# Kernel optimization log

Hardware: AMD Instinct MI355X
Metric: run time of the kernel (lower is better)

The kernel has to match this reference:

```python
import jax, jax.numpy as jnp
import numpy as np

N, E, HEADS = 50000, 800000, 4
IN_C, HID_C, OUT_C = 128, 64, 40
WIDTH = HEADS * HID_C  # 256
NEG_SLOPE = 0.2
BN_EPS = 1e-5


def setup_inputs() -> dict:
    key = jax.random.key(0)
    ks = jax.random.split(key, 16)
    s = 0.05
    inp = {
        "x": jax.random.normal(ks[0], (N, IN_C), jnp.float32),
        "edge_index": jax.random.randint(ks[1], (2, E), 0, N, jnp.int32),
        # layer 0: in -> (heads, hid), concat
        "W0": jax.random.normal(ks[2], (IN_C, WIDTH), jnp.float32) * s,
        "a_src0": jax.random.normal(ks[3], (HEADS, HID_C), jnp.float32) * s,
        "a_dst0": jax.random.normal(ks[4], (HEADS, HID_C), jnp.float32) * s,
        "b0": jnp.zeros((WIDTH,), jnp.float32),
        "g0": jnp.ones((WIDTH,), jnp.float32),
        "beta0": jnp.zeros((WIDTH,), jnp.float32),
        # layer 1: width -> (heads, hid), concat
        "W1": jax.random.normal(ks[5], (WIDTH, WIDTH), jnp.float32) * s,
        "a_src1": jax.random.normal(ks[6], (HEADS, HID_C), jnp.float32) * s,
        "a_dst1": jax.random.normal(ks[7], (HEADS, HID_C), jnp.float32) * s,
        "b1": jnp.zeros((WIDTH,), jnp.float32),
        "g1": jnp.ones((WIDTH,), jnp.float32),
        "beta1": jnp.zeros((WIDTH,), jnp.float32),
        # layer 2: width -> (heads, out), mean over heads (concat=False)
        "W2": jax.random.normal(ks[8], (WIDTH, HEADS * OUT_C), jnp.float32) * s,
        "a_src2": jax.random.normal(ks[9], (HEADS, OUT_C), jnp.float32) * s,
        "a_dst2": jax.random.normal(ks[10], (HEADS, OUT_C), jnp.float32) * s,
        "b2": jnp.zeros((OUT_C,), jnp.float32),
    }
    return inp


def _gat_layer(x, W, a_src, a_dst, b, src, dst, out_c, concat):
    # x: [N, F_in]; W: [F_in, HEADS*out_c]
    h = (x @ W).reshape(N, HEADS, out_c)              # [N, H, C]
    e_src = jnp.sum(h * a_src, axis=-1)               # [N, H]
    e_dst = jnp.sum(h * a_dst, axis=-1)               # [N, H]
    e = jax.nn.leaky_relu(e_src[src] + e_dst[dst], NEG_SLOPE)  # [E', H]
    # segment softmax over incoming edges of each destination node
    m = jax.ops.segment_max(e, dst, num_segments=N)
    e = jnp.exp(e - m[dst])
    z = jax.ops.segment_sum(e, dst, num_segments=N)
    alpha = e / (z[dst] + 1e-16)                      # [E', H]
    msg = h[src] * alpha[:, :, None]                  # [E', H, C]
    out = jax.ops.segment_sum(msg, dst, num_segments=N)  # [N, H, C]
    if concat:
        return out.reshape(N, HEADS * out_c) + b
    return out.mean(axis=1) + b


def _batchnorm(x, g, beta):
    mu = x.mean(axis=0)
    var = x.var(axis=0)
    return (x - mu) * jax.lax.rsqrt(var + BN_EPS) * g + beta


def reference(x, edge_index, W0, a_src0, a_dst0, b0, g0, beta0,
              W1, a_src1, a_dst1, b1, g1, beta1,
              W2, a_src2, a_dst2, b2):
    # add self-loops (PyG GATConv default)
    loops = jnp.arange(N, dtype=edge_index.dtype)
    src = jnp.concatenate([edge_index[0], loops])
    dst = jnp.concatenate([edge_index[1], loops])

    h = _gat_layer(x, W0, a_src0, a_dst0, b0, src, dst, HID_C, True)
    h = jax.nn.elu(_batchnorm(h, g0, beta0))
    h = _gat_layer(h, W1, a_src1, a_dst1, b1, src, dst, HID_C, True)
    h = jax.nn.elu(_batchnorm(h, g1, beta1))
    h = _gat_layer(h, W2, a_src2, a_dst2, b2, src, dst, OUT_C, False)
    return jax.nn.log_softmax(h, axis=-1)
```

## Files before the change

### kernel.cpp

```cpp
#include <hip/hip_runtime.h>

#define NN 50000
#define EE 800000
#define NEP (EE + NN)
#define NBS 512
#define SCB 49

typedef float f32x4 __attribute__((ext_vector_type(4)));
typedef float f32x2 __attribute__((ext_vector_type(2)));
typedef short bf16x8 __attribute__((ext_vector_type(8)));

__device__ inline float bf2f(unsigned short u) {
    union { unsigned int i; float f; } v; v.i = ((unsigned int)u) << 16; return v.f;
}
__device__ inline float lo2f(unsigned int u) {
    return __builtin_bit_cast(float, u << 16);
}
__device__ inline float hi2f(unsigned int u) {
    return __builtin_bit_cast(float, u & 0xFFFF0000u);
}
__device__ inline unsigned short f2bf(float f) {
    unsigned int x = __builtin_bit_cast(unsigned int, f);
    unsigned int r = x + 0x7FFFu + ((x >> 16) & 1u);
    return (unsigned short)(r >> 16);
}

__global__ __launch_bounds__(256) void k_cs(const int* __restrict__ ei,
                                            int* __restrict__ counts, int* __restrict__ lps) {
    int e = blockIdx.x * 256 + threadIdx.x;
    if (e >= NEP) return;
    int dst = (e < EE) ? ei[EE + e] : (e - EE);
    lps[e] = atomicAdd(&counts[dst], 1);
}

__global__ __launch_bounds__(256) void k_scan1(const int* __restrict__ counts,
                                               int* __restrict__ indptr, int* __restrict__ bsum) {
    const int tid = threadIdx.x, lane = tid & 63, wid = tid >> 6;
    const int base = blockIdx.x * 1024 + tid * 4;
    int4 v = make_int4(0, 0, 0, 0);
    if (base + 3 < NN) v = *(const int4*)&counts[base];
    else {
        if (base + 0 < NN) v.x = counts[base + 0];
        if (base + 1 < NN) v.y = counts[base + 1];
        if (base + 2 < NN) v.z = counts[base + 2];
        if (base + 3 < NN) v.w = counts[base + 3];
    }
    int t = v.x + v.y + v.z + v.w;
    int s = t;
    #pragma unroll
    for (int d = 1; d < 64; d <<= 1) { int u = __shfl_up(s, d); if (lane >= d) s += u; }
    __shared__ int ws[4], wo[4];
    if (lane == 63) ws[wid] = s;
    __syncthreads();
    if (tid == 0) {
        int a = 0;
        #pragma unroll
        for (int j = 0; j < 4; j++) { wo[j] = a; a += ws[j]; }
        bsum[blockIdx.x] = a;
    }
    __syncthreads();
    int excl = wo[wid] + s - t;
    int p0 = excl, p1 = p0 + v.x, p2 = p1 + v.y, p3 = p2 + v.z;
    if (base + 3 < NN) *(int4*)&indptr[base] = make_int4(p0, p1, p2, p3);
    else {
        if (base + 0 < NN) indptr[base + 0] = p0;
        if (base + 1 < NN) indptr[base + 1] = p1;
        if (base + 2 < NN) indptr[base + 2] = p2;
        if (base + 3 < NN) indptr[base + 3] = p3;
    }
}

__global__ __launch_bounds__(64) void k_scan2(int* __restrict__ bsum, int* __restrict__ indptr) {
    const int lane = threadIdx.x;
    int v = (lane < SCB) ? bsum[lane] : 0;
    int s = v;
    #pragma unroll
    for (int d = 1; d < 64; d <<= 1) { int u = __shfl_up(s, d); if (lane >= d) s += u; }
    if (lane < SCB) bsum[lane] = s - v;
    if (lane == SCB - 1) indptr[NN] = s;
}

__global__ __launch_bounds__(256) void k_scan3(int* __restrict__ indptr, const int* __restrict__ bsum) {
    const int base = blockIdx.x * 1024 + threadIdx.x * 4;
    const int off = bsum[blockIdx.x];
    if (off == 0) return;
    if (base + 3 < NN) {
        int4 v = *(const int4*)&indptr[base];
        v.x += off; v.y += off; v.z += off; v.w += off;
        *(int4*)&indptr[base] = v;
    } else {
        #pragma unroll
        for (int j = 0; j < 4; j++)
            if (base + j < NN) indptr[base + j] += off;
    }
}

__global__ __launch_bounds__(256) void k_place(const int* __restrict__ ei,
                                               const int* __restrict__ indptr,
                                               const int* __restrict__ lps,
                                               int* __restrict__ srcs) {
    int e = blockIdx.x * 256 + threadIdx.x;
    if (e >= NEP) return;
    int src, dst;
    if (e < EE) { src = ei[e]; dst = ei[EE + e]; }
    else        { src = e - EE; dst = src; }
    srcs[indptr[dst] + lps[e]] = src;
}

__global__ __launch_bounds__(256) void k_expand(const int* __restrict__ indptr,
                                                int* __restrict__ dstc) {
    const int wid = threadIdx.x >> 6, lane = threadIdx.x & 63;
    const int n = blockIdx.x * 4 + wid;
    if (n >= NN) return;
    const int e0 = __builtin_amdgcn_readfirstlane(indptr[n]);
    const int e1 = __builtin_amdgcn_readfirstlane(indptr[n + 1]);
    for (int e = e0 + lane; e < e1; e += 64) dstc[e] = n;
}

#define XN4 1600000
__global__ __launch_bounds__(256) void k_prep(const float* __restrict__ x, unsigned short* __restrict__ xb,
        const float* __restrict__ W0, unsigned short* __restrict__ Wt0,
        const float* __restrict__ W1, unsigned short* __restrict__ Wt1,
        const float* __restrict__ W2, unsigned short* __restrict__ Wt2,
        const float* __restrict__ vs0, const float* __restrict__ vd0,
        float4* __restrict__ es4, float4* __restrict__ ed4) {
    int i = blockIdx.x * 256 + threadIdx.x;
    if (i < XN4) {
        float4 v = ((const float4*)x)[i];
        ushort4 o;
        o.x = f2bf(v.x); o.y = f2bf(v.y); o.z = f2bf(v.z); o.w = f2bf(v.w);
        ((ushort4*)xb)[i] = o;
        const int k0 = (i & 31) * 4;
        const float vv[4] = {v.x, v.y, v.z, v.w};
        float s[4] = {0.f, 0.f, 0.f, 0.f}, dd[4] = {0.f, 0.f, 0.f, 0.f};
        #pragma unroll
        for (int j = 0; j < 4; j++) {
            float f = vv[j];
            float4 a = *(const float4*)&vs0[(k0 + j) * 4];
            float4 b = *(const float4*)&vd0[(k0 + j) * 4];
            s[0] += f * a.x; s[1] += f * a.y; s[2] += f * a.z; s[3] += f * a.w;
            dd[0] += f * b.x; dd[1] += f * b.y; dd[2] += f * b.z; dd[3] += f * b.w;
        }
        #pragma unroll
        for (int d = 1; d < 32; d <<= 1) {
            #pragma unroll
            for (int j = 0; j < 4; j++) { s[j] += __shfl_xor(s[j], d); dd[j] += __shfl_xor(dd[j], d); }
        }
        if ((threadIdx.x & 31) == 0) {
            int row = i >> 5;
            es4[row] = make_float4(s[0], s[1], s[2], s[3]);
            ed4[row] = make_float4(dd[0], dd[1], dd[2], dd[3]);
        }
        return;
    }
    i -= XN4;
    if (i < 256 * 128) {
        int c = i >> 7, k = i & 127;
        Wt0[i] = f2bf(W0[(size_t)k * 256 + c]);
        return;
    }
    i -= 256 * 128;
    if (i < 256 * 256) {
        int c = i >> 8, k = i & 255;
        Wt1[i] = f2bf(W1[(size_t)k * 256 + c]);
        return;
    }
    i -= 256 * 256;
    if (i < 192 * 256) {
        int c = i >> 8, k = i & 255;
        Wt2[i] = f2bf((c < 160) ? W2[(size_t)k * 160 + c] : 0.f);
    }
}

__global__ __launch_bounds__(256) void k_wv(
        const float* __restrict__ W0, const float* __restrict__ as0, const float* __restrict__ ad0,
        const float* __restrict__ W1, const float* __restrict__ as1, const float* __restrict__ ad1,
        const float* __restrict__ W2, const float* __restrict__ as2, const float* __restrict__ ad2,
        float* __restrict__ vs0, float* __restrict__ vd0,
        float* __restrict__ vs1, float* __restrict__ vd1,
        float* __restrict__ vs2, float* __restrict__ vd2) {
    int b = blockIdx.x;
    const float *W, *as_, *ad_; float *vs, *vd; int k, C, NO;
    if (b < 128)      { W = W0; as_ = as0; ad_ = ad0; vs = vs0; vd = vd0; k = b;       C = 64; NO = 256; }
    else if (b < 384) { W = W1; as_ = as1; ad_ = ad1; vs = vs1; vd = vd1; k = b - 128; C = 64; NO = 256; }
    else              { W = W2; as_ = as2; ad_ = ad2; vs = vs2; vd = vd2; k = b - 384; C = 40; NO = 160; }
    int h = threadIdx.x >> 6, c = threadIdx.x & 63;
    float s1 = 0.f, s2 = 0.f;
    if (c < C) {
        float wv = W[(size_t)k * NO + h * C + c];
        s1 = wv * as_[h * C + c];
        s2 = wv * ad_[h * C + c];
    }
    #pragma unroll
    for (int d = 1; d < 64; d <<= 1) { s1 += __shfl_xor(s1, d); s2 += __shfl_xor(s2, d); }
    if (c == 0) { vs[k * 4 + h] = s1; vd[k * 4 + h] = s2; }
}

__global__ __launch_bounds__(256) void k_wgt(const float4* __restrict__ es4,
        const float4* __restrict__ ed4, const int* __restrict__ srcs,
        const int* __restrict__ dstc, float* __restrict__ wqf) {
    int p = blockIdx.x * 256 + threadIdx.x;
    if (p >= NEP) return;
    float4 s = es4[srcs[p]];
    float4 d = ed4[dstc[p]];
    float e0 = s.x + d.x, e1 = s.y + d.y, e2 = s.z + d.z, e3 = s.w + d.w;
    e0 = (e0 > 0.f) ? e0 : 0.2f * e0;
    e1 = (e1 > 0.f) ? e1 : 0.2f * e1;
    e2 = (e2 > 0.f) ? e2 : 0.2f * e2;
    e3 = (e3 > 0.f) ? e3 : 0.2f * e3;
    wqf[p]            = __expf(e0);
    wqf[NEP + p]      = __expf(e1);
    wqf[2 * NEP + p]  = __expf(e2);
    wqf[3 * NEP + p]  = __expf(e3);
}

template<int K, int NOUTP, int NO>
__global__ __launch_bounds__(256) void k_gemm(const unsigned short* __restrict__ Xb,
                                              const unsigned short* __restrict__ Wt,
                                              unsigned char* __restrict__ Y) {
    constexpr int G = K / 8;
    __shared__ __attribute__((aligned(16))) unsigned short As[64 * K];
    const int bm = blockIdx.x * 64;
    const int tid = threadIdx.x, lane = tid & 63, wid = tid >> 6;
    const int wm = wid >> 1, wn = wid & 1;
    const int l15 = lane & 15, l4 = lane >> 4;

    #pragma unroll
    for (int i = 0; i < (64 * G) / 256; i++) {
        int p = tid + 256 * i;
        int row = p / G, g = p % G;
        int grow = bm + row; if (grow >= NN) grow = 0;
        int gsrc = g ^ (row & 7);
        const unsigned short* gp = &Xb[(size_t)grow * K + gsrc * 8];
        __builtin_amdgcn_global_load_lds(
            (const __attribute__((address_space(1))) void*)gp,
            (__attribute__((address_space(3))) void*)&As[p * 8],
            16, 0, 0);
    }
    __syncthreads();

    #pragma unroll
    for (int bg = 0; bg < NOUTP / 64; bg++) {
        const int bn = bg * 64;
        bf16x8 bfr[2][K / 32];
        #pragma unroll
        for (int n = 0; n < 2; n++) {
            const int col = bn + wn * 32 + n * 16 + l15;
            #pragma unroll
            for (int ks = 0; ks < K / 32; ks++)
                bfr[n][ks] = *(const bf16x8*)&Wt[(size_t)col * K + ks * 32 + l4 * 8];
        }
        f32x4 acc[2][2];
        #pragma unroll
        for (int m = 0; m < 2; m++)
            #pragma unroll
            for (int n = 0; n < 2; n++) acc[m][n] = (f32x4)0.f;
        #pragma unroll
        for (int ks = 0; ks < K / 32; ks++) {
            #pragma unroll
            for (int m = 0; m < 2; m++) {
                const int r = wm * 32 + m * 16 + l15;
                const int pg = ((ks << 2) + l4) ^ (r & 7);
                bf16x8 af = *(const bf16x8*)&As[r * K + pg * 8];
                #pragma unroll
                for (int n = 0; n < 2; n++)
                    acc[m][n] = __builtin_amdgcn_mfma_f32_16x16x32_bf16(af, bfr[n][ks], acc[m][n], 0, 0, 0);
            }
        }
        #pragma unroll
        for (int m = 0; m < 2; m++) {
            const int row0 = bm + wm * 32 + m * 16 + l4 * 4;
            #pragma unroll
            for (int n = 0; n < 2; n++) {
                const int col = bn + wn * 32 + n * 16 + l15;
                if (col >= NO) continue;
                #pragma unroll
                for (int j = 0; j < 4; j++) {
                    int gr = row0 + j;
                    if (gr >= NN) continue;
                    int pk = __builtin_amdgcn_cvt_pk_fp8_f32(acc[m][n][j], acc[m][n][j], 0, false);
                    Y[(size_t)gr * NOUTP + col] = (unsigned char)pk;
                }
            }
        }
    }
}

__global__ __launch_bounds__(256) void k_agg(const unsigned char* __restrict__ H,
        const float* __restrict__ wqf,
        const int* __restrict__ indptr, const int* __restrict__ srcs,
        unsigned short* __restrict__ outp) {
    const int wid = threadIdx.x >> 6, lane = threadIdx.x & 63;
    const int n = blockIdx.x * 4 + wid;
    if (n >= NN) return;
    const int head = lane >> 4;
    const float* __restrict__ wh = wqf + (size_t)head * NEP;
    const int e0 = __builtin_amdgcn_readfirstlane(indptr[n]);
    const int e1 = __builtin_amdgcn_readfirstlane(indptr[n + 1]);
    float z = 0.f, a0 = 0.f, a1 = 0.f, a2 = 0.f, a3 = 0.f;
    const unsigned char* Hp = H + lane * 4;
    int e = e0;
    for (; e + 8 <= e1; e += 8) {
        int s[8]; float ww[8];
        #pragma unroll
        for (int q = 0; q < 8; q++) { s[q] = srcs[e + q]; ww[q] = wh[e + q]; }
        #pragma unroll
        for (int q = 0; q < 8; q++) {
            unsigned int hv = *(const unsigned int*)(Hp + (size_t)s[q] * 256);
            z += ww[q];
            f32x2 lo = __builtin_amdgcn_cvt_pk_f32_fp8(hv, false);
            f32x2 hi = __builtin_amdgcn_cvt_pk_f32_fp8(hv, true);
            a0 += ww[q] * lo[0]; a1 += ww[q] * lo[1];
            a2 += ww[q] * hi[0]; a3 += ww[q] * hi[1];
        }
    }
    for (; e < e1; ++e) {
        int s0 = srcs[e];
        float w0 = wh[e];
        unsigned int hv = *(const unsigned int*)(Hp + (size_t)s0 * 256);
        z += w0;
        f32x2 lo = __builtin_amdgcn_cvt_pk_f32_fp8(hv, false);
        f32x2 hi = __builtin_amdgcn_cvt_pk_f32_fp8(hv, true);
        a0 += w0 * lo[0]; a1 += w0 * lo[1];
        a2 += w0 * hi[0]; a3 += w0 * hi[1];
    }
    float inv = 1.f / (z + 1e-16f);
    ushort4 o;
    o.x = f2bf(a0 * inv); o.y = f2bf(a1 * inv); o.z = f2bf(a2 * inv); o.w = f2bf(a3 * inv);
    *(ushort4*)&outp[(size_t)n * 256 + lane * 4] = o;
}

__global__ __launch_bounds__(256) void k_agg2(const unsigned char* __restrict__ H2,
        const float* __restrict__ wqf,
        const int* __restrict__ indptr, const int* __restrict__ srcs,
        const float* __restrict__ b2, float* __restrict__ outp) {
    const int wid = threadIdx.x >> 6, lane = threadIdx.x & 63;
    const int n = blockIdx.x * 4 + wid;
    if (n >= NN) return;
    const bool act = lane < 40;
    const int head = lane / 10;
    const float* __restrict__ wh = wqf + (size_t)(act ? head : 0) * NEP;
    const int e0 = __builtin_amdgcn_readfirstlane(indptr[n]);
    const int e1 = __builtin_amdgcn_readfirstlane(indptr[n + 1]);
    float z = 0.f, acc[4] = {0.f, 0.f, 0.f, 0.f};
    const unsigned char* Hp = H2 + lane * 4;
    if (act) {
        int e = e0;
        for (; e + 8 <= e1; e += 8) {
            int s[8]; float ww[8];
            #pragma unroll
            for (int q = 0; q < 8; q++) { s[q] = srcs[e + q]; ww[q] = wh[e + q]; }
            #pragma unroll
            for (int q = 0; q < 8; q++) {
                unsigned int hv = *(const unsigned int*)(Hp + (size_t)s[q] * 192);
                z += ww[q];
                f32x2 lo = __builtin_amdgcn_cvt_pk_f32_fp8(hv, false);
                f32x2 hi = __builtin_amdgcn_cvt_pk_f32_fp8(hv, true);
                acc[0] += ww[q] * lo[0]; acc[1] += ww[q] * lo[1];
                acc[2] += ww[q] * hi[0]; acc[3] += ww[q] * hi[1];
            }
        }
        for (; e < e1; ++e) {
            int s0 = srcs[e];
            float w0 = wh[e];
            unsigned int hv = *(const unsigned int*)(Hp + (size_t)s0 * 192);
            z += w0;
            f32x2 lo = __builtin_amdgcn_cvt_pk_f32_fp8(hv, false);
            f32x2 hi = __builtin_amdgcn_cvt_pk_f32_fp8(hv, true);
            acc[0] += w0 * lo[0]; acc[1] += w0 * lo[1];
            acc[2] += w0 * hi[0]; acc[3] += w0 * hi[1];
        }
    }
    float inv = 1.f / (z + 1e-16f);
    float sv[4];
    #pragma unroll
    for (int j = 0; j < 4; j++) sv[j] = acc[j] * inv;
    #pragma unroll
    for (int j = 0; j < 4; j++) {
        float v = sv[j];
        v += __shfl(sv[j], lane + 10);
        v += __shfl(sv[j], lane + 20);
        v += __shfl(sv[j], lane + 30);
        sv[j] = v;
    }
    const bool ol = lane < 10;
    float m4 = -1e30f;
    #pragma unroll
    for (int j = 0; j < 4; j++) {
        sv[j] = ol ? (0.25f * sv[j] + b2[lane * 4 + j]) : -1e30f;
        m4 = fmaxf(m4, sv[j]);
    }
    #pragma unroll
    for (int d = 1; d < 16; d <<= 1) m4 = fmaxf(m4, __shfl_xor(m4, d));
    float s = 0.f;
    #pragma unroll
    for (int j = 0; j < 4; j++) s += ol ? __expf(sv[j] - m4) : 0.f;
    #pragma unroll
    for (int d = 1; d < 16; d <<= 1) s += __shfl_xor(s, d);
    float ls = logf(s);
    if (ol) {
        float4 o = make_float4(sv[0] - m4 - ls, sv[1] - m4 - ls, sv[2] - m4 - ls, sv[3] - m4 - ls);
        *(float4*)&outp[(size_t)n * 40 + lane * 4] = o;
    }
}

__global__ __launch_bounds__(256) void k_bnstats1(const unsigned short* __restrict__ X,
        float* __restrict__ ps, float* __restrict__ pq) {
    __shared__ float lds[4 * 256];
    const int tid = threadIdx.x;
    const int colg = (tid & 63) * 4;
    const int w = tid >> 6;
    float s[4] = {0.f, 0.f, 0.f, 0.f}, q[4] = {0.f, 0.f, 0.f, 0.f};
    for (int r = blockIdx.x * 4 + w; r < NN; r += NBS * 4) {
        ushort4 hv = *(const ushort4*)&X[(size_t)r * 256 + colg];
        const unsigned short hh[4] = {hv.x, hv.y, hv.z, hv.w};
        #pragma unroll
        for (int j = 0; j < 4; j++) { float v = bf2f(hh[j]); s[j] += v; q[j] += v * v; }
    }
    #pragma unroll
    for (int j = 0; j < 4; j++) lds[w * 256 + colg + j] = s[j];
    __syncthreads();
    float ts = lds[tid] + lds[256 + tid] + lds[512 + tid] + lds[768 + tid];
    __syncthreads();
    #pragma unroll
    for (int j = 0; j < 4; j++) lds[w * 256 + colg + j] = q[j];
    __syncthreads();
    float tq = lds[tid] + lds[256 + tid] + lds[512 + tid] + lds[768 + tid];
    ps[(size_t)blockIdx.x * 256 + tid] = ts;
    pq[(size_t)blockIdx.x * 256 + tid] = tq;
}

__global__ __launch_bounds__(256) void k_bnred(const float* __restrict__ ps,
        const float* __restrict__ pq, const float* __restrict__ g,
        const float* __restrict__ beta, float* __restrict__ sc_o, float* __restrict__ sh_o) {
    const int col = blockIdx.x, tid = threadIdx.x;
    float s = ps[(size_t)tid * 256 + col] + ps[(size_t)(tid + 256) * 256 + col];
    float q = pq[(size_t)tid * 256 + col] + pq[(size_t)(tid + 256) * 256 + col];
    #pragma unroll
    for (int d = 1; d < 64; d <<= 1) { s += __shfl_xor(s, d); q += __shfl_xor(q, d); }
    __shared__ float ls[4], lq[4];
    if ((tid & 63) == 0) { ls[tid >> 6] = s; lq[tid >> 6] = q; }
    __syncthreads();
    if (tid == 0) {
        float S = ls[0] + ls[1] + ls[2] + ls[3];
        float Q = lq[0] + lq[1] + lq[2] + lq[3];
        const float inv = 1.f / (float)NN;
        float mu = S * inv;
        float var = Q * inv - mu * mu;
        float sc = rsqrtf(var + 1e-5f) * g[col];
        sc_o[col] = sc;
        sh_o[col] = beta[col] - mu * sc;
    }
}

__global__ __launch_bounds__(256) void k_bnapply(unsigned short* __restrict__ X,
        const float* __restrict__ sc_i, const float* __restrict__ sh_i,
        const float* __restrict__ vs, const float* __restrict__ vd,
        float4* __restrict__ es4, float4* __restrict__ ed4) {
    const int hl = threadIdx.x & 31;
    const int colg = hl * 8;
    const int rowo = threadIdx.x >> 5;
    float sc[8], sh[8];
    #pragma unroll
    for (int j = 0; j < 8; j++) { sc[j] = sc_i[colg + j]; sh[j] = sh_i[colg + j]; }
    for (int r = blockIdx.x * 8 + rowo; r < NN; r += gridDim.x * 8) {
        uint4 u = *(uint4*)&X[(size_t)r * 256 + colg];
        unsigned int uu[4] = {u.x, u.y, u.z, u.w};
        unsigned int oo[4];
        float s[4] = {0.f, 0.f, 0.f, 0.f}, dd[4] = {0.f, 0.f, 0.f, 0.f};
        #pragma unroll
        for (int p = 0; p < 4; p++) {
            float lo = lo2f(uu[p]);
            float hi = hi2f(uu[p]);
            float vlo = lo * sc[p * 2] + sh[p * 2];
            float vhi = hi * sc[p * 2 + 1] + sh[p * 2 + 1];
            vlo = (vlo > 0.f) ? vlo : expm1f(vlo);
            vhi = (vhi > 0.f) ? vhi : expm1f(vhi);
            oo[p] = (unsigned int)f2bf(vlo) | ((unsigned int)f2bf(vhi) << 16);
            float4 a0 = *(const float4*)&vs[(colg + 2 * p) * 4];
            float4 b0 = *(const float4*)&vd[(colg + 2 * p) * 4];
            float4 a1 = *(const float4*)&vs[(colg + 2 * p + 1) * 4];
            float4 b1 = *(const float4*)&vd[(colg + 2 * p + 1) * 4];
            s[0] += vlo * a0.x + vhi * a1.x; s[1] += vlo * a0.y + vhi * a1.y;
            s[2] += vlo * a0.z + vhi * a1.z; s[3] += vlo * a0.w + vhi * a1.w;
            dd[0] += vlo * b0.x + vhi * b1.x; dd[1] += vlo * b0.y + vhi * b1.y;
            dd[2] += vlo * b0.z + vhi * b1.z; dd[3] += vlo * b0.w + vhi * b1.w;
        }
        *(uint4*)&X[(size_t)r * 256 + colg] = make_uint4(oo[0], oo[1], oo[2], oo[3]);
        #pragma unroll
        for (int d = 1; d < 32; d <<= 1) {
            #pragma unroll
            for (int j = 0; j < 4; j++) { s[j] += __shfl_xor(s[j], d); dd[j] += __shfl_xor(dd[j], d); }
        }
        if (hl == 0) {
            es4[r] = make_float4(s[0], s[1], s[2], s[3]);
            ed4[r] = make_float4(dd[0], dd[1], dd[2], dd[3]);
        }
    }
}

extern "C" void kernel_launch(void* const* d_in, const int* in_sizes, int n_in,
                              void* d_out, int out_size, void* d_ws, size_t ws_size,
                              hipStream_t stream) {
    const float* x   = (const float*)d_in[0];
    const int*   ei  = (const int*)d_in[1];
    const float* W0  = (const float*)d_in[2];
    const float* as0 = (const float*)d_in[3];
    const float* ad0 = (const float*)d_in[4];
    const float* g0  = (const float*)d_in[6];
    const float* be0 = (const float*)d_in[7];
    const float* W1  = (const float*)d_in[8];
    const float* as1 = (const float*)d_in[9];
    const float* ad1 = (const float*)d_in[10];
    const float* g1  = (const float*)d_in[12];
    const float* be1 = (const float*)d_in[13];
    const float* W2  = (const float*)d_in[14];
    const float* as2 = (const float*)d_in[15];
    const float* ad2 = (const float*)d_in[16];
    const float* b2  = (const float*)d_in[17];
    float* out = (float*)d_out;

    char* w = (char*)d_ws;
    size_t off = 0;
    auto take = [&](size_t bytes) -> void* {
        off = (off + 255) & ~(size_t)255;
        void* p = w + off; off += bytes; return p;
    };
    unsigned short* Agg16 = (unsigned short*)take((size_t)NN * 256 * 2);
    unsigned short* xb    = (unsigned short*)take((size_t)NN * 128 * 2);
    unsigned char*  H8    = (unsigned char*)take((size_t)NN * 256);
    float* es     = (float*)take((size_t)NN * 4 * 4);
    float* ed     = (float*)take((size_t)NN * 4 * 4);
    int*   counts = (int*)take((size_t)NN * 4);
    int*   indptr = (int*)take((size_t)(NN + 1) * 4);
    int*   lps    = (int*)take((size_t)NEP * 4);
    int*   srcs   = (int*)take((size_t)NEP * 4);
    int*   dstc   = (int*)take((size_t)NEP * 4);
    float* wqf    = (float*)take((size_t)NEP * 4 * 4);
    int*   bsum   = (int*)take(64 * 4);
    unsigned short* Wt0 = (unsigned short*)take((size_t)256 * 128 * 2);
    unsigned short* Wt1 = (unsigned short*)take((size_t)256 * 256 * 2);
    unsigned short* Wt2 = (unsigned short*)take((size_t)192 * 256 * 2);
    float* vs0 = (float*)take(128 * 4 * 4);
    float* vd0 = (float*)take(128 * 4 * 4);
    float* vs1 = (float*)take(256 * 4 * 4);
    float* vd1 = (float*)take(256 * 4 * 4);
    float* vs2 = (float*)take(256 * 4 * 4);
    float* vd2 = (float*)take(256 * 4 * 4);
    float* ps  = (float*)take((size_t)NBS * 256 * 4);
    float* pq  = (float*)take((size_t)NBS * 256 * 4);
    float* bns = (float*)take(512 * 4);

    const int gE = (NEP + 255) / 256;
    const int gPrep = (XN4 + 256 * 128 + 256 * 256 + 192 * 256 + 255) / 256;

    k_wv<<<640, 256, 0, stream>>>(W0, as0, ad0, W1, as1, ad1, W2, as2, ad2,
                                  vs0, vd0, vs1, vd1, vs2, vd2);
    k_prep<<<gPrep, 256, 0, stream>>>(x, xb, W0, Wt0, W1, Wt1, W2, Wt2,
                                      vs0, vd0, (float4*)es, (float4*)ed);

    hipMemsetAsync(counts, 0, (size_t)NN * 4, stream);
    k_cs   <<<gE, 256, 0, stream>>>(ei, counts, lps);
    k_scan1<<<SCB, 256, 0, stream>>>(counts, indptr, bsum);
    k_scan2<<<1, 64, 0, stream>>>(bsum, indptr);
    k_scan3<<<SCB, 256, 0, stream>>>(indptr, bsum);
    k_place<<<gE, 256, 0, stream>>>(ei, indptr, lps, srcs);

    const int gM = (NN + 63) / 64;
    const int gW = (NN + 3) / 4;

    k_expand<<<gW, 256, 0, stream>>>(indptr, dstc);

    k_wgt<<<gE, 256, 0, stream>>>((const float4*)es, (const float4*)ed, srcs, dstc, wqf);
    k_gemm<128, 256, 256><<<gM, 256, 0, stream>>>(xb, Wt0, H8);
    k_agg<<<gW, 256, 0, stream>>>(H8, wqf, indptr, srcs, Agg16);
    k_bnstats1<<<NBS, 256, 0, stream>>>(Agg16, ps, pq);
    k_bnred<<<256, 256, 0, stream>>>(ps, pq, g0, be0, bns, bns + 256);
    k_bnapply<<<1024, 256, 0, stream>>>(Agg16, bns, bns + 256, vs1, vd1,
                                        (float4*)es, (float4*)ed);

    k_wgt<<<gE, 256, 0, stream>>>((const float4*)es, (const float4*)ed, srcs, dstc, wqf);
    k_gemm<256, 256, 256><<<gM, 256, 0, stream>>>(Agg16, Wt1, H8);
    k_agg<<<gW, 256, 0, stream>>>(H8, wqf, indptr, srcs, Agg16);
    k_bnstats1<<<NBS, 256, 0, stream>>>(Agg16, ps, pq);
    k_bnred<<<256, 256, 0, stream>>>(ps, pq, g1, be1, bns, bns + 256);
    k_bnapply<<<1024, 256, 0, stream>>>(Agg16, bns, bns + 256, vs2, vd2,
                                        (float4*)es, (float4*)ed);

    k_wgt<<<gE, 256, 0, stream>>>((const float4*)es, (const float4*)ed, srcs, dstc, wqf);
    k_gemm<256, 192, 160><<<gM, 256, 0, stream>>>(Agg16, Wt2, H8);
    k_agg2<<<gW, 256, 0, stream>>>(H8, wqf, indptr, srcs, b2, out);
}
```

Measured before the change: 381.5 us.

## Merge independent kernels via block-range dispatch and pack edge weights as bf16

```diff
diff --git a/kernel.cpp b/kernel.cpp
--- a/kernel.cpp
+++ b/kernel.cpp
@@ -25,12 +25,72 @@
     return (unsigned short)(r >> 16);
 }
 
-__global__ __launch_bounds__(256) void k_cs(const int* __restrict__ ei,
-                                            int* __restrict__ counts, int* __restrict__ lps) {
-    int e = blockIdx.x * 256 + threadIdx.x;
-    if (e >= NEP) return;
-    int dst = (e < EE) ? ei[EE + e] : (e - EE);
-    lps[e] = atomicAdd(&counts[dst], 1);
+#define XN4 1600000
+#define GPREP 6826
+#define GEDGE 3321
+#define GWAVE 12500
+#define GMAT  782
+
+__global__ __launch_bounds__(256) void k_prep(const float* __restrict__ x, unsigned short* __restrict__ xb,
+        const float* __restrict__ W0, unsigned short* __restrict__ Wt0,
+        const float* __restrict__ W1, unsigned short* __restrict__ Wt1,
+        const float* __restrict__ W2, unsigned short* __restrict__ Wt2,
+        const float* __restrict__ vs0, const float* __restrict__ vd0,
+        float4* __restrict__ es4, float4* __restrict__ ed4,
+        const int* __restrict__ ei, int* __restrict__ counts, int* __restrict__ lps) {
+    if (blockIdx.x >= GPREP) {
+        int e = (blockIdx.x - GPREP) * 256 + threadIdx.x;
+        if (e >= NEP) return;
+        int dst = (e < EE) ? ei[EE + e] : (e - EE);
+        lps[e] = atomicAdd(&counts[dst], 1);
+        return;
+    }
+    int i = blockIdx.x * 256 + threadIdx.x;
+    if (i < XN4) {
+        float4 v = ((const float4*)x)[i];
+        ushort4 o;
+        o.x = f2bf(v.x); o.y = f2bf(v.y); o.z = f2bf(v.z); o.w = f2bf(v.w);
+        ((ushort4*)xb)[i] = o;
+        const int k0 = (i & 31) * 4;
+        const float vv[4] = {v.x, v.y, v.z, v.w};
+        float s[4] = {0.f, 0.f, 0.f, 0.f}, dd[4] = {0.f, 0.f, 0.f, 0.f};
+        #pragma unroll
+        for (int j = 0; j < 4; j++) {
+            float f = vv[j];
+            float4 a = *(const float4*)&vs0[(k0 + j) * 4];
+            float4 b = *(const float4*)&vd0[(k0 + j) * 4];
+            s[0] += f * a.x; s[1] += f * a.y; s[2] += f * a.z; s[3] += f * a.w;
+            dd[0] += f * b.x; dd[1] += f * b.y; dd[2] += f * b.z; dd[3] += f * b.w;
+        }
+        #pragma unroll
+        for (int d = 1; d < 32; d <<= 1) {
+            #pragma unroll
+            for (int j = 0; j < 4; j++) { s[j] += __shfl_xor(s[j], d); dd[j] += __shfl_xor(dd[j], d); }
+        }
+        if ((threadIdx.x & 31) == 0) {
+            int row = i >> 5;
+            es4[row] = make_float4(s[0], s[1], s[2], s[3]);
+            ed4[row] = make_float4(dd[0], dd[1], dd[2], dd[3]);
+        }
+        return;
+    }
+    i -= XN4;
+    if (i < 256 * 128) {
+        int c = i >> 7, k = i & 127;
+        Wt0[i] = f2bf(W0[(size_t)k * 256 + c]);
+        return;
+    }
+    i -= 256 * 128;
+    if (i < 256 * 256) {
+        int c = i >> 8, k = i & 255;
+        Wt1[i] = f2bf(W1[(size_t)k * 256 + c]);
+        return;
+    }
+    i -= 256 * 256;
+    if (i < 192 * 256) {
+        int c = i >> 8, k = i & 255;
+        Wt2[i] = f2bf((c < 160) ? W2[(size_t)k * 160 + c] : 0.f);
+    }
 }
 
 __global__ __launch_bounds__(256) void k_scan1(const int* __restrict__ counts,
@@ -98,78 +158,23 @@
 __global__ __launch_bounds__(256) void k_place(const int* __restrict__ ei,
                                                const int* __restrict__ indptr,
                                                const int* __restrict__ lps,
-                                               int* __restrict__ srcs) {
-    int e = blockIdx.x * 256 + threadIdx.x;
-    if (e >= NEP) return;
-    int src, dst;
-    if (e < EE) { src = ei[e]; dst = ei[EE + e]; }
-    else        { src = e - EE; dst = src; }
-    srcs[indptr[dst] + lps[e]] = src;
-}
-
-__global__ __launch_bounds__(256) void k_expand(const int* __restrict__ indptr,
-                                                int* __restrict__ dstc) {
+                                               int* __restrict__ srcs,
+                                               int* __restrict__ dstc) {
+    if (blockIdx.x < GEDGE) {
+        int e = blockIdx.x * 256 + threadIdx.x;
+        if (e >= NEP) return;
+        int src, dst;
+        if (e < EE) { src = ei[e]; dst = ei[EE + e]; }
+        else        { src = e - EE; dst = src; }
+        srcs[indptr[dst] + lps[e]] = src;
+        return;
+    }
     const int wid = threadIdx.x >> 6, lane = threadIdx.x & 63;
-    const int n = blockIdx.x * 4 + wid;
+    const int n = (blockIdx.x - GEDGE) * 4 + wid;
     if (n >= NN) return;
     const int e0 = __builtin_amdgcn_readfirstlane(indptr[n]);
     const int e1 = __builtin_amdgcn_readfirstlane(indptr[n + 1]);
     for (int e = e0 + lane; e < e1; e += 64) dstc[e] = n;
-}
-
-#define XN4 1600000
-__global__ __launch_bounds__(256) void k_prep(const float* __restrict__ x, unsigned short* __restrict__ xb,
-        const float* __restrict__ W0, unsigned short* __restrict__ Wt0,
-        const float* __restrict__ W1, unsigned short* __restrict__ Wt1,
-        const float* __restrict__ W2, unsigned short* __restrict__ Wt2,
-        const float* __restrict__ vs0, const float* __restrict__ vd0,
-        float4* __restrict__ es4, float4* __restrict__ ed4) {
-    int i = blockIdx.x * 256 + threadIdx.x;
-    if (i < XN4) {
-        float4 v = ((const float4*)x)[i];
-        ushort4 o;
-        o.x = f2bf(v.x); o.y = f2bf(v.y); o.z = f2bf(v.z); o.w = f2bf(v.w);
-        ((ushort4*)xb)[i] = o;
-        const int k0 = (i & 31) * 4;
-        const float vv[4] = {v.x, v.y, v.z, v.w};
-        float s[4] = {0.f, 0.f, 0.f, 0.f}, dd[4] = {0.f, 0.f, 0.f, 0.f};
-        #pragma unroll
-        for (int j = 0; j < 4; j++) {
-            float f = vv[j];
-            float4 a = *(const float4*)&vs0[(k0 + j) * 4];
-            float4 b = *(const float4*)&vd0[(k0 + j) * 4];
-            s[0] += f * a.x; s[1] += f * a.y; s[2] += f * a.z; s[3] += f * a.w;
-            dd[0] += f * b.x; dd[1] += f * b.y; dd[2] += f * b.z; dd[3] += f * b.w;
-        }
-        #pragma unroll
-        for (int d = 1; d < 32; d <<= 1) {
-            #pragma unroll
-            for (int j = 0; j < 4; j++) { s[j] += __shfl_xor(s[j], d); dd[j] += __shfl_xor(dd[j], d); }
-        }
-        if ((threadIdx.x & 31) == 0) {
-            int row = i >> 5;
-            es4[row] = make_float4(s[0], s[1], s[2], s[3]);
-            ed4[row] = make_float4(dd[0], dd[1], dd[2], dd[3]);
-        }
-        return;
-    }
-    i -= XN4;
-    if (i < 256 * 128) {
-        int c = i >> 7, k = i & 127;
-        Wt0[i] = f2bf(W0[(size_t)k * 256 + c]);
-        return;
-    }
-    i -= 256 * 128;
-    if (i < 256 * 256) {
-        int c = i >> 8, k = i & 255;
-        Wt1[i] = f2bf(W1[(size_t)k * 256 + c]);
-        return;
-    }
-    i -= 256 * 256;
-    if (i < 192 * 256) {
-        int c = i >> 8, k = i & 255;
-        Wt2[i] = f2bf((c < 160) ? W2[(size_t)k * 160 + c] : 0.f);
-    }
 }
 
 __global__ __launch_bounds__(256) void k_wv(
@@ -196,28 +201,31 @@
     if (c == 0) { vs[k * 4 + h] = s1; vd[k * 4 + h] = s2; }
 }
 
-__global__ __launch_bounds__(256) void k_wgt(const float4* __restrict__ es4,
-        const float4* __restrict__ ed4, const int* __restrict__ srcs,
-        const int* __restrict__ dstc, float* __restrict__ wqf) {
-    int p = blockIdx.x * 256 + threadIdx.x;
-    if (p >= NEP) return;
-    float4 s = es4[srcs[p]];
-    float4 d = ed4[dstc[p]];
-    float e0 = s.x + d.x, e1 = s.y + d.y, e2 = s.z + d.z, e3 = s.w + d.w;
-    e0 = (e0 > 0.f) ? e0 : 0.2f * e0;
-    e1 = (e1 > 0.f) ? e1 : 0.2f * e1;
-    e2 = (e2 > 0.f) ? e2 : 0.2f * e2;
-    e3 = (e3 > 0.f) ? e3 : 0.2f * e3;
-    wqf[p]            = __expf(e0);
-    wqf[NEP + p]      = __expf(e1);
-    wqf[2 * NEP + p]  = __expf(e2);
-    wqf[3 * NEP + p]  = __expf(e3);
-}
-
 template<int K, int NOUTP, int NO>
 __global__ __launch_bounds__(256) void k_gemm(const unsigned short* __restrict__ Xb,
                                               const unsigned short* __restrict__ Wt,
-                                              unsigned char* __restrict__ Y) {
+                                              unsigned char* __restrict__ Y,
+                                              const float4* __restrict__ es4,
+                                              const float4* __restrict__ ed4,
+                                              const int* __restrict__ srcs,
+                                              const int* __restrict__ dstc,
+                                              uint2* __restrict__ wq) {
+    if (blockIdx.x >= GMAT) {
+        int p = (blockIdx.x - GMAT) * 256 + threadIdx.x;
+        if (p >= NEP) return;
+        float4 s = es4[srcs[p]];
+        float4 d = ed4[dstc[p]];
+        float e0 = s.x + d.x, e1 = s.y + d.y, e2 = s.z + d.z, e3 = s.w + d.w;
+        e0 = (e0 > 0.f) ? e0 : 0.2f * e0;
+        e1 = (e1 > 0.f) ? e1 : 0.2f * e1;
+        e2 = (e2 > 0.f) ? e2 : 0.2f * e2;
+        e3 = (e3 > 0.f) ? e3 : 0.2f * e3;
+        uint2 o;
+        o.x = (unsigned int)f2bf(__expf(e0)) | ((unsigned int)f2bf(__expf(e1)) << 16);
+        o.y = (unsigned int)f2bf(__expf(e2)) | ((unsigned int)f2bf(__expf(e3)) << 16);
+        wq[p] = o;
+        return;
+    }
     constexpr int G = K / 8;
     __shared__ __attribute__((aligned(16))) unsigned short As[64 * K];
     const int bm = blockIdx.x * 64;
@@ -287,14 +295,14 @@
 }
 
 __global__ __launch_bounds__(256) void k_agg(const unsigned char* __restrict__ H,
-        const float* __restrict__ wqf,
+        const uint2* __restrict__ wq,
         const int* __restrict__ indptr, const int* __restrict__ srcs,
         unsigned short* __restrict__ outp) {
     const int wid = threadIdx.x >> 6, lane = threadIdx.x & 63;
     const int n = blockIdx.x * 4 + wid;
     if (n >= NN) return;
     const int head = lane >> 4;
-    const float* __restrict__ wh = wqf + (size_t)head * NEP;
+    const int hw = head >> 1, hs = (head & 1) * 16;
     const int e0 = __builtin_amdgcn_readfirstlane(indptr[n]);
     const int e1 = __builtin_amdgcn_readfirstlane(indptr[n + 1]);
     float z = 0.f, a0 = 0.f, a1 = 0.f, a2 = 0.f, a3 = 0.f;
@@ -303,7 +311,12 @@
     for (; e + 8 <= e1; e += 8) {
         int s[8]; float ww[8];
         #pragma unroll
-        for (int q = 0; q < 8; q++) { s[q] = srcs[e + q]; ww[q] = wh[e + q]; }
+        for (int q = 0; q < 8; q++) {
+            s[q] = srcs[e + q];
+            uint2 w2 = wq[e + q];
+            unsigned int wsv = hw ? w2.y : w2.x;
+            ww[q] = bf2f((unsigned short)(wsv >> hs));
+        }
         #pragma unroll
         for (int q = 0; q < 8; q++) {
             unsigned int hv = *(const unsigned int*)(Hp + (size_t)s[q] * 256);
@@ -316,7 +329,9 @@
     }
     for (; e < e1; ++e) {
         int s0 = srcs[e];
-        float w0 = wh[e];
+        uint2 w2 = wq[e];
+        unsigned int wsv = hw ? w2.y : w2.x;
+        float w0 = bf2f((unsigned short)(wsv >> hs));
         unsigned int hv = *(const unsigned int*)(Hp + (size_t)s0 * 256);
         z += w0;
         f32x2 lo = __builtin_amdgcn_cvt_pk_f32_fp8(hv, false);
@@ -331,7 +346,7 @@
 }
 
 __global__ __launch_bounds__(256) void k_agg2(const unsigned char* __restrict__ H2,
-        const float* __restrict__ wqf,
+        const uint2* __restrict__ wq,
         const int* __restrict__ indptr, const int* __restrict__ srcs,
         const float* __restrict__ b2, float* __restrict__ outp) {
     const int wid = threadIdx.x >> 6, lane = threadIdx.x & 63;
@@ -339,7 +354,7 @@
     if (n >= NN) return;
     const bool act = lane < 40;
     const int head = lane / 10;
-    const float* __restrict__ wh = wqf + (size_t)(act ? head : 0) * NEP;
+    const int hw = head >> 1, hs = (head & 1) * 16;
     const int e0 = __builtin_amdgcn_readfirstlane(indptr[n]);
     const int e1 = __builtin_amdgcn_readfirstlane(indptr[n + 1]);
     float z = 0.f, acc[4] = {0.f, 0.f, 0.f, 0.f};
@@ -349,7 +364,12 @@
         for (; e + 8 <= e1; e += 8) {
             int s[8]; float ww[8];
             #pragma unroll
-            for (int q = 0; q < 8; q++) { s[q] = srcs[e + q]; ww[q] = wh[e + q]; }
+            for (int q = 0; q < 8; q++) {
+                s[q] = srcs[e + q];
+                uint2 w2 = wq[e + q];
+                unsigned int wsv = hw ? w2.y : w2.x;
+                ww[q] = bf2f((unsigned short)(wsv >> hs));
+            }
             #pragma unroll
             for (int q = 0; q < 8; q++) {
                 unsigned int hv = *(const unsigned int*)(Hp + (size_t)s[q] * 192);
@@ -362,7 +382,9 @@
         }
         for (; e < e1; ++e) {
             int s0 = srcs[e];
-            float w0 = wh[e];
+            uint2 w2 = wq[e];
+            unsigned int wsv = hw ? w2.y : w2.x;
+            float w0 = bf2f((unsigned short)(wsv >> hs));
             unsigned int hv = *(const unsigned int*)(Hp + (size_t)s0 * 192);
             z += w0;
             f32x2 lo = __builtin_amdgcn_cvt_pk_f32_fp8(hv, false);
@@ -536,7 +558,7 @@
     int*   lps    = (int*)take((size_t)NEP * 4);
     int*   srcs   = (int*)take((size_t)NEP * 4);
     int*   dstc   = (int*)take((size_t)NEP * 4);
-    float* wqf    = (float*)take((size_t)NEP * 4 * 4);
+    uint2* wq     = (uint2*)take((size_t)NEP * 8);
     int*   bsum   = (int*)take(64 * 4);
     unsigned short* Wt0 = (unsigned short*)take((size_t)256 * 128 * 2);
     unsigned short* Wt1 = (unsigned short*)take((size_t)256 * 256 * 2);
@@ -551,43 +573,34 @@
     float* pq  = (float*)take((size_t)NBS * 256 * 4);
     float* bns = (float*)take(512 * 4);
 
-    const int gE = (NEP + 255) / 256;
-    const int gPrep = (XN4 + 256 * 128 + 256 * 256 + 192 * 256 + 255) / 256;
-
     k_wv<<<640, 256, 0, stream>>>(W0, as0, ad0, W1, as1, ad1, W2, as2, ad2,
                                   vs0, vd0, vs1, vd1, vs2, vd2);
-    k_prep<<<gPrep, 256, 0, stream>>>(x, xb, W0, Wt0, W1, Wt1, W2, Wt2,
-                                      vs0, vd0, (float4*)es, (float4*)ed);
-
     hipMemsetAsync(counts, 0, (size_t)NN * 4, stream);
-    k_cs   <<<gE, 256, 0, stream>>>(ei, counts, lps);
+    k_prep<<<GPREP + GEDGE, 256, 0, stream>>>(x, xb, W0, Wt0, W1, Wt1, W2, Wt2,
+                                              vs0, vd0, (float4*)es, (float4*)ed,
+                                              ei, counts, lps);
     k_scan1<<<SCB, 256, 0, stream>>>(counts, indptr, bsum);
     k_scan2<<<1, 64, 0, stream>>>(bsum, indptr);
     k_scan3<<<SCB, 256, 0, stream>>>(indptr, bsum);
-    k_place<<<gE, 256, 0, stream>>>(ei, indptr, lps, srcs);
-
-    const int gM = (NN + 63) / 64;
-    const int gW = (NN + 3) / 4;
-
-    k_expand<<<gW, 256, 0, stream>>>(indptr, dstc);
-
-    k_wgt<<<gE, 256, 0, stream>>>((const float4*)es, (const float4*)ed, srcs, dstc, wqf);
-    k_gemm<128, 256, 256><<<gM, 256, 0, stream>>>(xb, Wt0, H8);
-    k_agg<<<gW, 256, 0, stream>>>(H8, wqf, indptr, srcs, Agg16);
+    k_place<<<GEDGE + GWAVE, 256, 0, stream>>>(ei, indptr, lps, srcs, dstc);
+
+    k_gemm<128, 256, 256><<<GMAT + GEDGE, 256, 0, stream>>>(xb, Wt0, H8,
+            (const float4*)es, (const float4*)ed, srcs, dstc, wq);
+    k_agg<<<GWAVE, 256, 0, stream>>>(H8, wq, indptr, srcs, Agg16);
     k_bnstats1<<<NBS, 256, 0, stream>>>(Agg16, ps, pq);
     k_bnred<<<256, 256, 0, stream>>>(ps, pq, g0, be0, bns, bns + 256);
     k_bnapply<<<1024, 256, 0, stream>>>(Agg16, bns, bns + 256, vs1, vd1,
                                         (float4*)es, (float4*)ed);
 
-    k_wgt<<<gE, 256, 0, stream>>>((const float4*)es, (const float4*)ed, srcs, dstc, wqf);
-    k_gemm<256, 256, 256><<<gM, 256, 0, stream>>>(Agg16, Wt1, H8);
-    k_agg<<<gW, 256, 0, stream>>>(H8, wqf, indptr, srcs, Agg16);
+    k_gemm<256, 256, 256><<<GMAT + GEDGE, 256, 0, stream>>>(Agg16, Wt1, H8,
+            (const float4*)es, (const float4*)ed, srcs, dstc, wq);
+    k_agg<<<GWAVE, 256, 0, stream>>>(H8, wq, indptr, srcs, Agg16);
     k_bnstats1<<<NBS, 256, 0, stream>>>(Agg16, ps, pq);
     k_bnred<<<256, 256, 0, stream>>>(ps, pq, g1, be1, bns, bns + 256);
     k_bnapply<<<1024, 256, 0, stream>>>(Agg16, bns, bns + 256, vs2, vd2,
                                         (float4*)es, (float4*)ed);
 
-    k_wgt<<<gE, 256, 0, stream>>>((const float4*)es, (const float4*)ed, srcs, dstc, wqf);
-    k_gemm<256, 192, 160><<<gM, 256, 0, stream>>>(Agg16, Wt2, H8);
-    k_agg2<<<gW, 256, 0, stream>>>(H8, wqf, indptr, srcs, b2, out);
-}
+    k_gemm<256, 192, 160><<<GMAT + GEDGE, 256, 0, stream>>>(Agg16, Wt2, H8,
+            (const float4*)es, (const float4*)ed, srcs, dstc, wq);
+    k_agg2<<<GWAVE, 256, 0, stream>>>(H8, wq, indptr, srcs, b2, out);
+}
```

After: 352.2 us. 1.08x faster.
